# Kernel optimization log

Measured on AMD Instinct MI355X. Metric: run time of the kernel, lower is better.

The kernel has to match this reference:

```python
import jax, jax.numpy as jnp
from jax import lax
import numpy as np

UNITS, S, B, T = 64, 16, 512, 4096
LOG_2PI = float(np.log(2.0 * np.pi))


def setup_inputs() -> dict:
    key = jax.random.key(0)
    k1, k2 = jax.random.split(key)
    inputs = jax.random.normal(k1, (B, T), dtype=jnp.float32)
    # positive 'probs' (TFP Categorical takes log internally)
    hmm_params = jax.random.uniform(k2, (UNITS, S, S), dtype=jnp.float32,
                                    minval=1e-3, maxval=1.0)
    return {"inputs": inputs, "hmm_params": hmm_params}


def reference(inputs, hmm_params):
    # --- HMM parameters, as TFP builds them ---
    trans = hmm_params[0]                      # (S, S) unnormalized probs
    log_A = jnp.log(trans) - jnp.log(trans.sum(-1, keepdims=True))  # (S,S) row-normalized
    init = hmm_params[0, 0]                    # (S,)
    log_pi = jnp.log(init) - jnp.log(init.sum())
    # Emission: Normal(loc=0, scale=1) per state -> same logp for every state
    emit = -0.5 * inputs * inputs - 0.5 * LOG_2PI   # [B, T]
    emit = emit[:, :, None]                          # [B, T, 1] broadcasts over S

    # --- Viterbi forward (max-product) ---
    delta0 = log_pi[None, :] + emit[:, 0]            # [B, S]
    emit_seq = jnp.moveaxis(emit[:, 1:], 1, 0)       # [T-1, B, 1]

    def step(delta, e_t):
        scores = delta[:, :, None] + log_A[None, :, :]   # [B, S_prev, S_cur]
        psi = jnp.argmax(scores, axis=1).astype(jnp.int32)  # [B, S]
        delta_new = jnp.max(scores, axis=1) + e_t            # [B, S]
        return delta_new, psi

    deltaT, psis = lax.scan(step, delta0, emit_seq)  # psis: [T-1, B, S]

    # --- Backtrace ---
    zT = jnp.argmax(deltaT, axis=-1).astype(jnp.int32)   # [B]

    def back(z, psi):
        z_prev = jnp.take_along_axis(psi, z[:, None], axis=1)[:, 0]
        return z_prev, z_prev

    _, zs = lax.scan(back, zT, psis, reverse=True)   # zs: [T-1, B] = states t=0..T-2
    path = jnp.concatenate([zs.T, zT[:, None]], axis=1)  # [B, T]
    return path
```

## Files before the change

### kernel.cpp

```cpp
#include <hip/hip_runtime.h>
#include <math.h>

#define T_LEN 4096
#define B_SZ  512

__device__ __forceinline__ float emis(float xv) {
    float a = __fmul_rn(-0.5f, xv);
    float b = __fmul_rn(a, xv);
    return __fsub_rn(b, (float)0.9189385332046727);
}

__global__ __launch_bounds__(256) void k_emit(const float* __restrict__ x,
                                              float* __restrict__ Epad,
                                              float* __restrict__ E0,
                                              const float* __restrict__ hmm,
                                              float* __restrict__ logA,
                                              float* __restrict__ logAT) {
    int tid = threadIdx.x;
    if (blockIdx.x == 0) {
        int i = tid >> 4, j = tid & 15;
        const float* row = hmm + i * 16;
        float r[8];
#pragma unroll
        for (int k = 0; k < 8; ++k) r[k] = __fadd_rn(row[k], row[k + 8]);
        float s = __fadd_rn(
            __fadd_rn(__fadd_rn(r[0], r[1]), __fadd_rn(r[2], r[3])),
            __fadd_rn(__fadd_rn(r[4], r[5]), __fadd_rn(r[6], r[7])));
        float la = (float)log((double)row[j]);
        float ls = (float)log((double)s);
        float v = __fsub_rn(la, ls);
        logA[tid] = v;
        logAT[j * 16 + i] = v;
    }
    int i = blockIdx.x * 256 + tid;
    const float4* x4 = (const float4*)x;
    float4 xa = x4[i];
    float4 xb = (i + 1 < (B_SZ * T_LEN / 4)) ? x4[i + 1] : xa;
    float4 e;
    e.x = emis(xa.y); e.y = emis(xa.z); e.z = emis(xa.w); e.w = emis(xb.x);
    ((float4*)Epad)[i] = e;
    if ((i & 1023) == 0) E0[i >> 10] = emis(xa.x);
}

#define DPP_ROR0(K, SRC) __builtin_amdgcn_update_dpp(0, (SRC), 0x120 + (K), 0xF, 0xF, false)
#define M3(x, y, z) fmaxf(fmaxf(x, y), z)

#define ADDPP(DST, K)                                                                 \
    asm("v_add_f32_dpp %0, %1, %2 row_ror:" #K " row_mask:0xf bank_mask:0xf"          \
        : "=v"(DST) : "v"(d), "v"(a[K]))

#define STEPC(ET)                                                                     \
    {                                                                                 \
        float s0 = __fadd_rn(d, a[0]);                                                \
        float s1, s2, s3, s4, s5, s6, s7, s8, s9, s10, s11, s12, s13, s14, s15;       \
        ADDPP(s1, 1);   ADDPP(s2, 2);   ADDPP(s3, 3);   ADDPP(s4, 4);                 \
        ADDPP(s5, 5);   ADDPP(s6, 6);   ADDPP(s7, 7);   ADDPP(s8, 8);                 \
        ADDPP(s9, 9);   ADDPP(s10, 10); ADDPP(s11, 11); ADDPP(s12, 12);               \
        ADDPP(s13, 13); ADDPP(s14, 14); ADDPP(s15, 15);                               \
        float u0 = M3(s0, s1, s2),  u1 = M3(s3, s4, s5),  u2 = M3(s6, s7, s8);        \
        float u3 = M3(s9, s10, s11), u4 = M3(s12, s13, s14);                          \
        float m = fmaxf(M3(u0, u1, u2), M3(u3, u4, s15));                             \
        d = __fadd_rn(m, ET);                                                         \
    }

#define GRP4(QV, SLOTDW)                                                              \
    {                                                                                 \
        float4 dq;                                                                    \
        STEPC(QV.x) dq.x = d; STEPC(QV.y) dq.y = d;                                   \
        STEPC(QV.z) dq.z = d; STEPC(QV.w) dq.w = d;                                   \
        *(float4*)(db + (SLOTDW)) = dq;                                               \
    }

#define PERMSEL(V, Q)                                                                 \
    {                                                                                 \
        int sel_ = (V) & 7;                                                           \
        int lo_, hi_;                                                                 \
        asm("v_perm_b32 %0, %1, %2, %3" : "=v"(lo_) : "v"((Q).y), "v"((Q).x), "v"(sel_)); \
        asm("v_perm_b32 %0, %1, %2, %3" : "=v"(hi_) : "v"((Q).w), "v"((Q).z), "v"(sel_)); \
        V = (((V) & 8) ? hi_ : lo_) & 0xff;                                           \
    }

#define WALK64(BASE, CUR, PRE, POST)                                                  \
    {                                                                                 \
        uint4 m_[8];                                                                  \
        _Pragma("unroll") for (int z_ = 0; z_ < 8; ++z_)                              \
            m_[z_] = *(const uint4*)((BASE) + (63 - z_) * 16);                        \
        for (int r_ = 63; r_ >= 15; r_ -= 8) {                                        \
            uint4 n_[8];                                                              \
            _Pragma("unroll") for (int z_ = 0; z_ < 8; ++z_)                          \
                n_[z_] = *(const uint4*)((BASE) + (r_ - 8 - z_) * 16);                \
            _Pragma("unroll") for (int z_ = 0; z_ < 8; ++z_) {                        \
                PRE(r_ - z_, CUR) PERMSEL(CUR, m_[z_]) POST(r_ - z_, CUR)             \
            }                                                                         \
            _Pragma("unroll") for (int z_ = 0; z_ < 8; ++z_) m_[z_] = n_[z_];         \
        }                                                                             \
        _Pragma("unroll") for (int z_ = 0; z_ < 8; ++z_) {                            \
            PRE(7 - z_, CUR) PERMSEL(CUR, m_[z_]) POST(7 - z_, CUR)                   \
        }                                                                             \
    }

#define NOPX(r, c)
#define EBL_PRE(r, c) Ebl[r] = (unsigned char)(c);
#define OUT_POST(r, c) ob[r] = (c);

__global__ __launch_bounds__(256) void k_main(const float* __restrict__ Epad,
                                              const float* __restrict__ E0,
                                              const float* __restrict__ logA,
                                              const float* __restrict__ logAT,
                                              unsigned char* __restrict__ psi,
                                              unsigned char* __restrict__ M,
                                              float* __restrict__ carry) {
    __shared__ __align__(16) float dbuf[2][2][16][68];
    __shared__ uint4 pbufv[2][2][65];
    const int tid = threadIdx.x;
    const int wave = tid >> 6;
    const int blk = blockIdx.x;

    if (wave == 0) {
        asm volatile("s_setprio 3");
        const int j = tid & 15, g = tid >> 4;
        float a[16];
        float d = 0.f;
        float4 q0, q1, q2, q3;
        const float4* ep4 = nullptr;
        int b = 0;
        if (g < 2) {
            b = blk * 2 + g;
            a[0] = logA[j * 16 + j];
#define LOADA(K) { int sk = DPP_ROR0(K, j); a[K] = logA[sk * 16 + j]; }
            LOADA(1)  LOADA(2)  LOADA(3)  LOADA(4)  LOADA(5)
            LOADA(6)  LOADA(7)  LOADA(8)  LOADA(9)  LOADA(10)
            LOADA(11) LOADA(12) LOADA(13) LOADA(14) LOADA(15)
#undef LOADA
            ep4 = (const float4*)(Epad + (size_t)b * T_LEN);
            d = __fadd_rn(logA[j], E0[b]);
            q0 = ep4[0]; q1 = ep4[1]; q2 = ep4[2]; q3 = ep4[3];
        }
        for (int p = 0; p < 66; ++p) {
            __syncthreads();
            if (p < 64 && g < 2) {
                float* db = &dbuf[p & 1][g][j][0];
                db[64] = d;
                const float4* epc = ep4 + 16 * p;
                if (p < 63) {
#pragma clang loop unroll(disable)
                    for (int ii = 0; ii < 4; ++ii) {
                        GRP4(q0, ii * 16 + 0)  q0 = epc[(ii + 1) * 4 + 0];
                        GRP4(q1, ii * 16 + 4)  q1 = epc[(ii + 1) * 4 + 1];
                        GRP4(q2, ii * 16 + 8)  q2 = epc[(ii + 1) * 4 + 2];
                        GRP4(q3, ii * 16 + 12) q3 = epc[(ii + 1) * 4 + 3];
                    }
                } else {
#pragma clang loop unroll(disable)
                    for (int ii = 0; ii < 3; ++ii) {
                        GRP4(q0, ii * 16 + 0)  q0 = epc[(ii + 1) * 4 + 0];
                        GRP4(q1, ii * 16 + 4)  q1 = epc[(ii + 1) * 4 + 1];
                        GRP4(q2, ii * 16 + 8)  q2 = epc[(ii + 1) * 4 + 2];
                        GRP4(q3, ii * 16 + 12) q3 = epc[(ii + 1) * 4 + 3];
                    }
                    GRP4(q0, 48) GRP4(q1, 52) GRP4(q2, 56)
                    STEPC(q3.x) db[60] = d;
                    STEPC(q3.y) db[61] = d;
                    STEPC(q3.z) db[62] = d;
                }
            }
        }
        if (g < 2) carry[b * 16 + j] = d;
    } else if (wave <= 2) {
        const int g2 = wave - 1;
        const int r = tid & 63;
        const int b2 = blk * 2 + g2;
        for (int p = 0; p < 66; ++p) {
            __syncthreads();
            const int c = p - 1;
            if (c >= 0 && c < 64) {
                const int t2 = 64 * c + 1 + r;
                if (t2 <= T_LEN - 1) {
                    const int q = c & 1;
                    const int rs = (r == 0) ? 64 : (r - 1);
                    float dd[16];
#pragma unroll
                    for (int i = 0; i < 16; ++i) dd[i] = dbuf[q][g2][i][rs];
                    unsigned long long pk = 0ull;
#pragma clang loop unroll(disable)
                    for (int jj = 0; jj < 16; ++jj) {
                        const float* col = logAT + (jj << 4);
                        float best = __fadd_rn(dd[0], col[0]);
                        int arg = 0;
#pragma unroll
                        for (int i = 1; i < 16; ++i) {
                            float s = __fadd_rn(dd[i], col[i]);
                            if (s > best) arg = i;
                            best = fmaxf(best, s);
                        }
                        pk |= (unsigned long long)arg << (jj * 4);
                    }
                    unsigned w[4];
#pragma unroll
                    for (int qq = 0; qq < 4; ++qq) {
                        unsigned h = (unsigned)(pk >> (16 * qq)) & 0xFFFFu;
                        w[qq] = (h & 0xFu) | ((h & 0xF0u) << 4) |
                                ((h & 0xF00u) << 8) | ((h & 0xF000u) << 12);
                    }
                    uint4 pv = make_uint4(w[0], w[1], w[2], w[3]);
                    pbufv[q][g2][r] = pv;
                    *(uint4*)(psi + ((size_t)b2 * T_LEN + t2) * 16) = pv;
                }
            }
        }
    } else {
        const int l = tid - 192;
        const int g3 = l >> 4, z = l & 15;
        for (int p = 0; p < 66; ++p) {
            __syncthreads();
            const int c = p - 2;
            if (c >= 0 && l < 32) {
                const int cq = c & 1;
                if (c == 63)
                    ((unsigned char*)&pbufv[cq][g3][63])[z] = (unsigned char)z;
                asm volatile("" ::: "memory");
                const unsigned char* base = (const unsigned char*)&pbufv[cq][g3][0];
                int cur = z;
                WALK64(base, cur, NOPX, NOPX)
                M[((size_t)(blk * 2 + g3) * 64 + c) * 16 + z] = (unsigned char)cur;
            }
        }
    }
}

__global__ __launch_bounds__(256) void k_back(const unsigned char* __restrict__ psi,
                                              const float* __restrict__ carry,
                                              const unsigned char* __restrict__ M,
                                              int* __restrict__ out) {
    __shared__ uint4 bufv[64 * 65];
    __shared__ uint4 Mlv[64];
    __shared__ unsigned char Ebl[64];
    unsigned char* bufb = (unsigned char*)bufv;
    unsigned char* Ml = (unsigned char*)Mlv;
    const int b = blockIdx.x, tid = threadIdx.x;

    const uint4* src = (const uint4*)(psi + (size_t)b * T_LEN * 16 + 16);
    for (int k = tid; k < T_LEN - 1; k += 256)
        *(uint4*)(bufb + (k >> 6) * 1040 + (k & 63) * 16) = src[k];
    if (tid == 255)
        *(uint4*)(bufb + 63 * 1040 + 63 * 16) =
            make_uint4(0x03020100u, 0x07060504u, 0x0B0A0908u, 0x0F0E0D0Cu);
    if (tid < 64) Mlv[tid] = ((const uint4*)(M + (size_t)b * 1024))[tid];
    __syncthreads();

    if (tid == 0) {
        const float* dT = carry + b * 16;
        float best = dT[0]; int zT = 0;
#pragma unroll
        for (int i = 1; i < 16; ++i) {
            float s = dT[i];
            if (s > best) zT = i;
            best = fmaxf(best, s);
        }
        int z = zT;
        WALK64(Ml, z, EBL_PRE, NOPX)
    }
    __syncthreads();

    if (tid < 64) {
        const unsigned char* base = bufb + tid * 1040;
        int* ob = out + (size_t)b * T_LEN + tid * 64;
        int cur = Ebl[tid];
        WALK64(base, cur, NOPX, OUT_POST)
    }
}

extern "C" void kernel_launch(void* const* d_in, const int* in_sizes, int n_in,
                              void* d_out, int out_size, void* d_ws, size_t ws_size,
                              hipStream_t stream) {
    (void)in_sizes; (void)n_in; (void)out_size; (void)ws_size;
    const float* x   = (const float*)d_in[0];
    const float* hmm = (const float*)d_in[1];
    int* out = (int*)d_out;

    char* w = (char*)d_ws;
    float* logA  = (float*)w;
    float* logAT = (float*)(w + 1024);
    float* E0    = (float*)(w + 2048);
    float* carry = (float*)(w + 4096);
    unsigned char* psi = (unsigned char*)(w + 4096 + 32768);
    unsigned char* M   = psi + (size_t)B_SZ * T_LEN * 16;
    float* Epad = (float*)(M + (size_t)B_SZ * 64 * 16);

    hipLaunchKernelGGL(k_emit, dim3((B_SZ * T_LEN / 4) / 256), dim3(256), 0, stream,
                       x, Epad, E0, hmm, logA, logAT);

    hipLaunchKernelGGL(k_main, dim3(B_SZ / 2), dim3(256), 0, stream,
                       Epad, E0, logA, logAT, psi, M, carry);

    hipLaunchKernelGGL(k_back, dim3(B_SZ), dim3(256), 0, stream,
                       psi, carry, M, out);
}
```

Before: 312.8 us.

## Fuse backtrace into main kernel, keep nibble-packed psi in LDS

```diff
diff --git a/kernel.cpp b/kernel.cpp
--- a/kernel.cpp
+++ b/kernel.cpp
@@ -99,19 +99,40 @@
         }                                                                             \
     }
 
+#define NIBHOP(V, Q) (V) = (int)(((Q) >> ((unsigned)(V) << 2)) & 15ull);
+
+#define NWALK64(BASE, CUR, POST)                                                      \
+    {                                                                                 \
+        const unsigned long long* bb_ = (BASE);                                       \
+        unsigned long long m_[8];                                                     \
+        _Pragma("unroll") for (int z_ = 0; z_ < 8; ++z_) m_[z_] = bb_[63 - z_];       \
+        for (int r_ = 63; r_ >= 15; r_ -= 8) {                                       \
+            unsigned long long n_[8];                                                 \
+            _Pragma("unroll") for (int z_ = 0; z_ < 8; ++z_) n_[z_] = bb_[r_ - 8 - z_]; \
+            _Pragma("unroll") for (int z_ = 0; z_ < 8; ++z_) {                        \
+                NIBHOP(CUR, m_[z_]) POST(r_ - z_, CUR)                                \
+            }                                                                         \
+            _Pragma("unroll") for (int z_ = 0; z_ < 8; ++z_) m_[z_] = n_[z_];         \
+        }                                                                             \
+        _Pragma("unroll") for (int z_ = 0; z_ < 8; ++z_) {                            \
+            NIBHOP(CUR, m_[z_]) POST(7 - z_, CUR)                                     \
+        }                                                                             \
+    }
+
 #define NOPX(r, c)
-#define EBL_PRE(r, c) Ebl[r] = (unsigned char)(c);
+#define EBL_PRE(r, c) eb[r] = (unsigned char)(c);
 #define OUT_POST(r, c) ob[r] = (c);
 
 __global__ __launch_bounds__(256) void k_main(const float* __restrict__ Epad,
                                               const float* __restrict__ E0,
                                               const float* __restrict__ logA,
                                               const float* __restrict__ logAT,
-                                              unsigned char* __restrict__ psi,
-                                              unsigned char* __restrict__ M,
-                                              float* __restrict__ carry) {
+                                              int* __restrict__ out) {
     __shared__ __align__(16) float dbuf[2][2][16][68];
-    __shared__ uint4 pbufv[2][2][65];
+    __shared__ unsigned long long pnib[2][64 * 65];
+    __shared__ uint4 Mlv[2][64];
+    __shared__ unsigned char Ebl[2][64];
+    __shared__ float carry_l[2][16];
     const int tid = threadIdx.x;
     const int wave = tid >> 6;
     const int blk = blockIdx.x;
@@ -123,9 +144,8 @@
         float d = 0.f;
         float4 q0, q1, q2, q3;
         const float4* ep4 = nullptr;
-        int b = 0;
         if (g < 2) {
-            b = blk * 2 + g;
+            int b = blk * 2 + g;
             a[0] = logA[j * 16 + j];
 #define LOADA(K) { int sk = DPP_ROR0(K, j); a[K] = logA[sk * 16 + j]; }
             LOADA(1)  LOADA(2)  LOADA(3)  LOADA(4)  LOADA(5)
@@ -165,11 +185,10 @@
                 }
             }
         }
-        if (g < 2) carry[b * 16 + j] = d;
+        if (g < 2) carry_l[g][j] = d;
     } else if (wave <= 2) {
         const int g2 = wave - 1;
         const int r = tid & 63;
-        const int b2 = blk * 2 + g2;
         for (int p = 0; p < 66; ++p) {
             __syncthreads();
             const int c = p - 1;
@@ -195,16 +214,9 @@
                         }
                         pk |= (unsigned long long)arg << (jj * 4);
                     }
-                    unsigned w[4];
-#pragma unroll
-                    for (int qq = 0; qq < 4; ++qq) {
-                        unsigned h = (unsigned)(pk >> (16 * qq)) & 0xFFFFu;
-                        w[qq] = (h & 0xFu) | ((h & 0xF0u) << 4) |
-                                ((h & 0xF00u) << 8) | ((h & 0xF000u) << 12);
-                    }
-                    uint4 pv = make_uint4(w[0], w[1], w[2], w[3]);
-                    pbufv[q][g2][r] = pv;
-                    *(uint4*)(psi + ((size_t)b2 * T_LEN + t2) * 16) = pv;
+                    pnib[g2][c * 65 + r] = pk;
+                } else {
+                    pnib[g2][c * 65 + 63] = 0xFEDCBA9876543210ull;
                 }
             }
         }
@@ -215,58 +227,33 @@
             __syncthreads();
             const int c = p - 2;
             if (c >= 0 && l < 32) {
-                const int cq = c & 1;
-                if (c == 63)
-                    ((unsigned char*)&pbufv[cq][g3][63])[z] = (unsigned char)z;
-                asm volatile("" ::: "memory");
-                const unsigned char* base = (const unsigned char*)&pbufv[cq][g3][0];
                 int cur = z;
-                WALK64(base, cur, NOPX, NOPX)
-                M[((size_t)(blk * 2 + g3) * 64 + c) * 16 + z] = (unsigned char)cur;
+                NWALK64(&pnib[g3][c * 65], cur, NOPX)
+                ((unsigned char*)&Mlv[g3][c])[z] = (unsigned char)cur;
             }
         }
     }
-}
-
-__global__ __launch_bounds__(256) void k_back(const unsigned char* __restrict__ psi,
-                                              const float* __restrict__ carry,
-                                              const unsigned char* __restrict__ M,
-                                              int* __restrict__ out) {
-    __shared__ uint4 bufv[64 * 65];
-    __shared__ uint4 Mlv[64];
-    __shared__ unsigned char Ebl[64];
-    unsigned char* bufb = (unsigned char*)bufv;
-    unsigned char* Ml = (unsigned char*)Mlv;
-    const int b = blockIdx.x, tid = threadIdx.x;
-
-    const uint4* src = (const uint4*)(psi + (size_t)b * T_LEN * 16 + 16);
-    for (int k = tid; k < T_LEN - 1; k += 256)
-        *(uint4*)(bufb + (k >> 6) * 1040 + (k & 63) * 16) = src[k];
-    if (tid == 255)
-        *(uint4*)(bufb + 63 * 1040 + 63 * 16) =
-            make_uint4(0x03020100u, 0x07060504u, 0x0B0A0908u, 0x0F0E0D0Cu);
-    if (tid < 64) Mlv[tid] = ((const uint4*)(M + (size_t)b * 1024))[tid];
+
     __syncthreads();
-
-    if (tid == 0) {
-        const float* dT = carry + b * 16;
-        float best = dT[0]; int zT = 0;
+    if (tid < 2) {
+        const int g = tid;
+        float best = carry_l[g][0]; int zT = 0;
 #pragma unroll
         for (int i = 1; i < 16; ++i) {
-            float s = dT[i];
+            float s = carry_l[g][i];
             if (s > best) zT = i;
             best = fmaxf(best, s);
         }
         int z = zT;
-        WALK64(Ml, z, EBL_PRE, NOPX)
+        unsigned char* eb = &Ebl[g][0];
+        WALK64((const unsigned char*)&Mlv[g][0], z, EBL_PRE, NOPX)
     }
     __syncthreads();
-
-    if (tid < 64) {
-        const unsigned char* base = bufb + tid * 1040;
-        int* ob = out + (size_t)b * T_LEN + tid * 64;
-        int cur = Ebl[tid];
-        WALK64(base, cur, NOPX, OUT_POST)
+    if (tid < 128) {
+        const int g = tid >> 6, c = tid & 63;
+        int* ob = out + (size_t)(blk * 2 + g) * T_LEN + c * 64;
+        int cur = Ebl[g][c];
+        NWALK64(&pnib[g][c * 65], cur, OUT_POST)
     }
 }
 
@@ -282,17 +269,11 @@
     float* logA  = (float*)w;
     float* logAT = (float*)(w + 1024);
     float* E0    = (float*)(w + 2048);
-    float* carry = (float*)(w + 4096);
-    unsigned char* psi = (unsigned char*)(w + 4096 + 32768);
-    unsigned char* M   = psi + (size_t)B_SZ * T_LEN * 16;
-    float* Epad = (float*)(M + (size_t)B_SZ * 64 * 16);
+    float* Epad  = (float*)(w + 4096);
 
     hipLaunchKernelGGL(k_emit, dim3((B_SZ * T_LEN / 4) / 256), dim3(256), 0, stream,
                        x, Epad, E0, hmm, logA, logAT);
 
     hipLaunchKernelGGL(k_main, dim3(B_SZ / 2), dim3(256), 0, stream,
-                       Epad, E0, logA, logAT, psi, M, carry);
-
-    hipLaunchKernelGGL(k_back, dim3(B_SZ), dim3(256), 0, stream,
-                       psi, carry, M, out);
-}
+                       Epad, E0, logA, logAT, out);
+}
```

Result: faster. 306.3 us (-2.1%).
